# Kernel optimization log

Hardware: AMD Instinct MI355X
Metric: run time of the kernel (lower is better)

Reference implementation:

```python
import jax, jax.numpy as jnp
import numpy as np

N_SOURCE, N_TARGET, D, TFD, E = 100000, 50000, 128, 32, 640000


def setup_inputs() -> dict:
    key = jax.random.key(0)
    ks = jax.random.split(key, 6)
    x = jax.random.normal(ks[0], (N_SOURCE, D), dtype=jnp.float32)
    conv_weight = jax.random.normal(ks[1], (D, D), dtype=jnp.float32) / np.sqrt(D)
    conv_bias = jax.random.normal(ks[2], (D,), dtype=jnp.float32)
    target_feat = jax.random.normal(ks[3], (N_TARGET, TFD), dtype=jnp.float32)
    edge_weight = jax.random.uniform(ks[4], (E,), dtype=jnp.float32)
    inter_edge_index = jax.random.randint(ks[5], (2, E), 0, N_TARGET, dtype=jnp.int64)
    return {
        "x": x,
        "conv_weight": conv_weight,
        "conv_bias": conv_bias,
        "target_feat": target_feat,
        "edge_weight": edge_weight,
        "inter_edge_index": inter_edge_index,
    }


def reference(x, conv_weight, conv_bias, target_feat, edge_weight, inter_edge_index):
    n_source, _ = x.shape
    n_target = target_feat.shape[0]
    n_nodes = n_source + n_target  # padded graph: [source ; zero target rows]
    row = inter_edge_index[0]                 # source node ids
    col = inter_edge_index[1] + n_source      # shifted target node ids

    # GCN linear transform (zero-padded target rows stay zero, so only transform x)
    h = x @ conv_weight  # [n_source, D]

    # gcn_norm with remaining self-loops (fill value 1): deg = scatter_add over row + 1
    deg = jax.ops.segment_sum(edge_weight, row, num_segments=n_nodes) + 1.0
    dinv = jnp.where(deg > 0, jax.lax.rsqrt(deg), 0.0)
    norm = dinv[row] * edge_weight * dinv[col]  # [E]

    # message = norm * h[row]; aggregate (add) at targets. Self-loop messages on
    # targets are zero (zero-padded features), so they are omitted.
    msg = norm[:, None] * h[row]                       # [E, D]
    out_t = jax.ops.segment_sum(msg, col - n_source, num_segments=n_target)
    out_t = out_t + conv_bias

    out_t = jax.nn.relu(out_t)                         # if_relu=True
    return jnp.concatenate([out_t, jnp.abs(target_feat)], axis=1)  # mod='cat'
```

## Files before the change

### kernel.cpp

```cpp
#include <hip/hip_runtime.h>

#define N_SOURCE 100000
#define N_TARGET 50000
#define DIM 128
#define TFD 32
#define NE 640000
#define CAP 64

typedef __attribute__((ext_vector_type(8))) short short8;
typedef __attribute__((ext_vector_type(4))) float f32x4;

static constexpr size_t DEG_OFF   = 0;
static constexpr size_t CNT_OFF   = 262144;
static constexpr size_t XBF_OFF   = 524288;
static constexpr size_t WT_OFF    = 13324288;
static constexpr size_t PAIRS_OFF = 13357056;
static constexpr size_t ACC_OFF   = 26157056;

__device__ __forceinline__ unsigned short f2bf(float f) {
  unsigned u = __float_as_uint(f);
  return (unsigned short)((u + 0x7FFFu + ((u >> 16) & 1u)) >> 16);
}
__device__ __forceinline__ float bf2f(unsigned short u) {
  return __uint_as_float(((unsigned)u) << 16);
}

#define PREP_X_BLOCKS 3125
#define PREP_W_BLOCKS 8
#define EDGE_BLOCKS 2500
#define TOTAL_BLOCKS (PREP_X_BLOCKS + PREP_W_BLOCKS + EDGE_BLOCKS)

__global__ void prep_edges(const float* __restrict__ x, const float* __restrict__ W,
                           const int* __restrict__ row, const int* __restrict__ col,
                           const float* __restrict__ ew,
                           unsigned short* __restrict__ xbf, unsigned short* __restrict__ wt,
                           float* __restrict__ deg, int* __restrict__ cnt,
                           int* __restrict__ pairs) {
  int b = blockIdx.x, tid = threadIdx.x;
  if (b < PREP_X_BLOCKS) {
    size_t t = (size_t)b * 256 + tid;
    const float4* x4 = (const float4*)x;
    float4 u = x4[2 * t], v = x4[2 * t + 1];
    ((ushort4*)xbf)[2 * t]     = make_ushort4(f2bf(u.x), f2bf(u.y), f2bf(u.z), f2bf(u.w));
    ((ushort4*)xbf)[2 * t + 1] = make_ushort4(f2bf(v.x), f2bf(v.y), f2bf(v.z), f2bf(v.w));
  } else if (b < PREP_X_BLOCKS + PREP_W_BLOCKS) {
    int t = (b - PREP_X_BLOCKS) * 2048 + tid * 8;
    int n = t >> 7, k0 = t & 127;
#pragma unroll
    for (int j = 0; j < 8; ++j)
      wt[n * 128 + k0 + j] = f2bf(W[(k0 + j) * 128 + n]);
  } else {
    int e = (b - PREP_X_BLOCKS - PREP_W_BLOCKS) * 256 + tid;
    if (e >= NE) return;
    int c = col[e];
    int pos = atomicAdd(&cnt[c], 1);
    if (pos < CAP) pairs[(size_t)c * CAP + pos] = e;
    atomicAdd(&deg[row[e]], ew[e]);
  }
}

__global__ __launch_bounds__(256) void gather_agg(const int* __restrict__ cnt,
                                                  const int* __restrict__ pairs,
                                                  const float* __restrict__ deg,
                                                  const int* __restrict__ row,
                                                  const float* __restrict__ ew,
                                                  const unsigned short* __restrict__ xbf,
                                                  unsigned short* __restrict__ accb) {
  int g = blockIdx.x * 8 + (threadIdx.x >> 5);
  int lane = threadIdx.x & 31;
  if (g >= N_TARGET) return;
  int n = cnt[g];
  if (n > CAP) n = CAP;
  const int* __restrict__ pb = pairs + (size_t)g * CAP;
  float4 s = {0.f, 0.f, 0.f, 0.f};
  int e = 0;
  for (; e + 4 <= n; e += 4) {
    int4 q = *(const int4*)(pb + e);
    int r0 = row[q.x], r1 = row[q.y], r2 = row[q.z], r3 = row[q.w];
    float n0 = rsqrtf(deg[r0] + 1.0f) * ew[q.x];
    float n1 = rsqrtf(deg[r1] + 1.0f) * ew[q.y];
    float n2 = rsqrtf(deg[r2] + 1.0f) * ew[q.z];
    float n3 = rsqrtf(deg[r3] + 1.0f) * ew[q.w];
    ushort4 a0 = *(const ushort4*)(xbf + (size_t)r0 * DIM + lane * 4);
    ushort4 a1 = *(const ushort4*)(xbf + (size_t)r1 * DIM + lane * 4);
    ushort4 a2 = *(const ushort4*)(xbf + (size_t)r2 * DIM + lane * 4);
    ushort4 a3 = *(const ushort4*)(xbf + (size_t)r3 * DIM + lane * 4);
    s.x = fmaf(n0, bf2f(a0.x), s.x); s.y = fmaf(n0, bf2f(a0.y), s.y);
    s.z = fmaf(n0, bf2f(a0.z), s.z); s.w = fmaf(n0, bf2f(a0.w), s.w);
    s.x = fmaf(n1, bf2f(a1.x), s.x); s.y = fmaf(n1, bf2f(a1.y), s.y);
    s.z = fmaf(n1, bf2f(a1.z), s.z); s.w = fmaf(n1, bf2f(a1.w), s.w);
    s.x = fmaf(n2, bf2f(a2.x), s.x); s.y = fmaf(n2, bf2f(a2.y), s.y);
    s.z = fmaf(n2, bf2f(a2.z), s.z); s.w = fmaf(n2, bf2f(a2.w), s.w);
    s.x = fmaf(n3, bf2f(a3.x), s.x); s.y = fmaf(n3, bf2f(a3.y), s.y);
    s.z = fmaf(n3, bf2f(a3.z), s.z); s.w = fmaf(n3, bf2f(a3.w), s.w);
  }
  for (; e < n; ++e) {
    int pe = pb[e];
    int r = row[pe];
    float nr = rsqrtf(deg[r] + 1.0f) * ew[pe];
    ushort4 a = *(const ushort4*)(xbf + (size_t)r * DIM + lane * 4);
    s.x = fmaf(nr, bf2f(a.x), s.x); s.y = fmaf(nr, bf2f(a.y), s.y);
    s.z = fmaf(nr, bf2f(a.z), s.z); s.w = fmaf(nr, bf2f(a.w), s.w);
  }
  *(ushort4*)(accb + (size_t)g * DIM + lane * 4) =
      make_ushort4(f2bf(s.x), f2bf(s.y), f2bf(s.z), f2bf(s.w));
}

__global__ __launch_bounds__(256) void gemm_mfma(
    const unsigned short* __restrict__ accb, const unsigned short* __restrict__ wt,
    const float* __restrict__ bias, const float* __restrict__ tf,
    float* __restrict__ out) {
  const int tid = threadIdx.x;
  const int wave = tid >> 6;
  const int lane = tid & 63;
  const int row0 = blockIdx.x * 64;

  {
    const float4* tf4 = (const float4*)tf;
    int base = blockIdx.x * 512 + tid * 2;
#pragma unroll
    for (int q = 0; q < 2; ++q) {
      int t = base + q;
      int i = t >> 3, j = t & 7;
      if (i < N_TARGET) {
        float4 v = tf4[t];
        v.x = fabsf(v.x); v.y = fabsf(v.y); v.z = fabsf(v.z); v.w = fabsf(v.w);
        ((float4*)(out + (size_t)i * (DIM + TFD) + DIM))[j] = v;
      }
    }
  }

  const int mrow = row0 + wave * 16 + (lane & 15);
  const int kg = lane >> 4;
  short8 a[4];
  {
    const unsigned short* ap = accb + (size_t)mrow * DIM + kg * 8;
#pragma unroll
    for (int t = 0; t < 4; ++t) a[t] = *(const short8*)(ap + t * 32);
  }

  const int ncol = lane & 15;
  const int orow0 = row0 + wave * 16 + (lane >> 4) * 4;
#pragma unroll
  for (int c = 0; c < 8; ++c) {
    int n = c * 16 + ncol;
    f32x4 acc = {0.f, 0.f, 0.f, 0.f};
    const unsigned short* bp = wt + (size_t)n * DIM + kg * 8;
#pragma unroll
    for (int t = 0; t < 4; ++t) {
      short8 b = *(const short8*)(bp + t * 32);
      acc = __builtin_amdgcn_mfma_f32_16x16x32_bf16(a[t], b, acc, 0, 0, 0);
    }
    float bv = bias[n];
#pragma unroll
    for (int r = 0; r < 4; ++r) {
      int i = orow0 + r;
      if (i < N_TARGET)
        out[(size_t)i * (DIM + TFD) + n] = fmaxf(acc[r] + bv, 0.f);
    }
  }
}

extern "C" void kernel_launch(void* const* d_in, const int* in_sizes, int n_in,
                              void* d_out, int out_size, void* d_ws, size_t ws_size,
                              hipStream_t stream) {
  const float* x    = (const float*)d_in[0];
  const float* W    = (const float*)d_in[1];
  const float* bias = (const float*)d_in[2];
  const float* tf   = (const float*)d_in[3];
  const float* ew   = (const float*)d_in[4];
  const int*   eidx = (const int*)d_in[5];
  const int* row = eidx;
  const int* col = eidx + NE;
  float* out = (float*)d_out;

  float*          deg   = (float*)((char*)d_ws + DEG_OFF);
  int*            cnt   = (int*)((char*)d_ws + CNT_OFF);
  unsigned short* xbf   = (unsigned short*)((char*)d_ws + XBF_OFF);
  unsigned short* wt    = (unsigned short*)((char*)d_ws + WT_OFF);
  int*            pairs = (int*)((char*)d_ws + PAIRS_OFF);
  unsigned short* accb  = (unsigned short*)((char*)d_ws + ACC_OFF);

  hipMemsetAsync(d_ws, 0, XBF_OFF, stream);

  prep_edges<<<TOTAL_BLOCKS, 256, 0, stream>>>(x, W, row, col, ew, xbf, wt, deg, cnt, pairs);
  gather_agg<<<(N_TARGET + 7) / 8, 256, 0, stream>>>(cnt, pairs, deg, row, ew, xbf, accb);
  gemm_mfma<<<(N_TARGET + 63) / 64, 256, 0, stream>>>(accb, wt, bias, tf, out);
}
```

Baseline: 235.5 us.

## Fuse prep, gather and GEMM into one cooperative persistent kernel

```diff
diff --git a/kernel.cpp b/kernel.cpp
--- a/kernel.cpp
+++ b/kernel.cpp
@@ -1,4 +1,7 @@
 #include <hip/hip_runtime.h>
+#include <hip/hip_cooperative_groups.h>
+
+namespace cg = cooperative_groups;
 
 #define N_SOURCE 100000
 #define N_TARGET 50000
@@ -6,12 +9,15 @@
 #define TFD 32
 #define NE 640000
 #define CAP 64
+#define NBLK 1024
+#define NTHR 256
+#define NT (NBLK * NTHR)
 
 typedef __attribute__((ext_vector_type(8))) short short8;
 typedef __attribute__((ext_vector_type(4))) float f32x4;
 
 static constexpr size_t DEG_OFF   = 0;
-static constexpr size_t CNT_OFF   = 262144;
+static constexpr size_t CNT_OFF   = 204800;
 static constexpr size_t XBF_OFF   = 524288;
 static constexpr size_t WT_OFF    = 13324288;
 static constexpr size_t PAIRS_OFF = 13357056;
@@ -25,33 +31,28 @@
   return __uint_as_float(((unsigned)u) << 16);
 }
 
-#define PREP_X_BLOCKS 3125
-#define PREP_W_BLOCKS 8
-#define EDGE_BLOCKS 2500
-#define TOTAL_BLOCKS (PREP_X_BLOCKS + PREP_W_BLOCKS + EDGE_BLOCKS)
-
-__global__ void prep_edges(const float* __restrict__ x, const float* __restrict__ W,
-                           const int* __restrict__ row, const int* __restrict__ col,
-                           const float* __restrict__ ew,
-                           unsigned short* __restrict__ xbf, unsigned short* __restrict__ wt,
-                           float* __restrict__ deg, int* __restrict__ cnt,
-                           int* __restrict__ pairs) {
-  int b = blockIdx.x, tid = threadIdx.x;
-  if (b < PREP_X_BLOCKS) {
-    size_t t = (size_t)b * 256 + tid;
-    const float4* x4 = (const float4*)x;
+
+__device__ __forceinline__ void phase_prep_edges(
+    int gt, const float* __restrict__ x, const float* __restrict__ W,
+    const int* __restrict__ row, const int* __restrict__ col,
+    const float* __restrict__ ew, unsigned short* __restrict__ xbf,
+    unsigned short* __restrict__ wt, float* __restrict__ deg,
+    int* __restrict__ cnt, int* __restrict__ pairs) {
+  const float4* x4 = (const float4*)x;
+  ushort4* xb4 = (ushort4*)xbf;
+  for (int t = gt; t < 800000; t += NT) {
     float4 u = x4[2 * t], v = x4[2 * t + 1];
-    ((ushort4*)xbf)[2 * t]     = make_ushort4(f2bf(u.x), f2bf(u.y), f2bf(u.z), f2bf(u.w));
-    ((ushort4*)xbf)[2 * t + 1] = make_ushort4(f2bf(v.x), f2bf(v.y), f2bf(v.z), f2bf(v.w));
-  } else if (b < PREP_X_BLOCKS + PREP_W_BLOCKS) {
-    int t = (b - PREP_X_BLOCKS) * 2048 + tid * 8;
+    xb4[2 * t]     = make_ushort4(f2bf(u.x), f2bf(u.y), f2bf(u.z), f2bf(u.w));
+    xb4[2 * t + 1] = make_ushort4(f2bf(v.x), f2bf(v.y), f2bf(v.z), f2bf(v.w));
+  }
+  if (gt < 2048) {
+    int t = gt * 8;
     int n = t >> 7, k0 = t & 127;
 #pragma unroll
     for (int j = 0; j < 8; ++j)
       wt[n * 128 + k0 + j] = f2bf(W[(k0 + j) * 128 + n]);
-  } else {
-    int e = (b - PREP_X_BLOCKS - PREP_W_BLOCKS) * 256 + tid;
-    if (e >= NE) return;
+  }
+  for (int e = gt; e < NE; e += NT) {
     int c = col[e];
     int pos = atomicAdd(&cnt[c], 1);
     if (pos < CAP) pairs[(size_t)c * CAP + pos] = e;
@@ -59,106 +60,137 @@
   }
 }
 
-__global__ __launch_bounds__(256) void gather_agg(const int* __restrict__ cnt,
-                                                  const int* __restrict__ pairs,
-                                                  const float* __restrict__ deg,
-                                                  const int* __restrict__ row,
-                                                  const float* __restrict__ ew,
-                                                  const unsigned short* __restrict__ xbf,
-                                                  unsigned short* __restrict__ accb) {
-  int g = blockIdx.x * 8 + (threadIdx.x >> 5);
-  int lane = threadIdx.x & 31;
-  if (g >= N_TARGET) return;
-  int n = cnt[g];
-  if (n > CAP) n = CAP;
-  const int* __restrict__ pb = pairs + (size_t)g * CAP;
-  float4 s = {0.f, 0.f, 0.f, 0.f};
-  int e = 0;
-  for (; e + 4 <= n; e += 4) {
-    int4 q = *(const int4*)(pb + e);
-    int r0 = row[q.x], r1 = row[q.y], r2 = row[q.z], r3 = row[q.w];
-    float n0 = rsqrtf(deg[r0] + 1.0f) * ew[q.x];
-    float n1 = rsqrtf(deg[r1] + 1.0f) * ew[q.y];
-    float n2 = rsqrtf(deg[r2] + 1.0f) * ew[q.z];
-    float n3 = rsqrtf(deg[r3] + 1.0f) * ew[q.w];
-    ushort4 a0 = *(const ushort4*)(xbf + (size_t)r0 * DIM + lane * 4);
-    ushort4 a1 = *(const ushort4*)(xbf + (size_t)r1 * DIM + lane * 4);
-    ushort4 a2 = *(const ushort4*)(xbf + (size_t)r2 * DIM + lane * 4);
-    ushort4 a3 = *(const ushort4*)(xbf + (size_t)r3 * DIM + lane * 4);
-    s.x = fmaf(n0, bf2f(a0.x), s.x); s.y = fmaf(n0, bf2f(a0.y), s.y);
-    s.z = fmaf(n0, bf2f(a0.z), s.z); s.w = fmaf(n0, bf2f(a0.w), s.w);
-    s.x = fmaf(n1, bf2f(a1.x), s.x); s.y = fmaf(n1, bf2f(a1.y), s.y);
-    s.z = fmaf(n1, bf2f(a1.z), s.z); s.w = fmaf(n1, bf2f(a1.w), s.w);
-    s.x = fmaf(n2, bf2f(a2.x), s.x); s.y = fmaf(n2, bf2f(a2.y), s.y);
-    s.z = fmaf(n2, bf2f(a2.z), s.z); s.w = fmaf(n2, bf2f(a2.w), s.w);
-    s.x = fmaf(n3, bf2f(a3.x), s.x); s.y = fmaf(n3, bf2f(a3.y), s.y);
-    s.z = fmaf(n3, bf2f(a3.z), s.z); s.w = fmaf(n3, bf2f(a3.w), s.w);
-  }
-  for (; e < n; ++e) {
-    int pe = pb[e];
-    int r = row[pe];
-    float nr = rsqrtf(deg[r] + 1.0f) * ew[pe];
-    ushort4 a = *(const ushort4*)(xbf + (size_t)r * DIM + lane * 4);
-    s.x = fmaf(nr, bf2f(a.x), s.x); s.y = fmaf(nr, bf2f(a.y), s.y);
-    s.z = fmaf(nr, bf2f(a.z), s.z); s.w = fmaf(nr, bf2f(a.w), s.w);
-  }
-  *(ushort4*)(accb + (size_t)g * DIM + lane * 4) =
-      make_ushort4(f2bf(s.x), f2bf(s.y), f2bf(s.z), f2bf(s.w));
-}
-
-__global__ __launch_bounds__(256) void gemm_mfma(
-    const unsigned short* __restrict__ accb, const unsigned short* __restrict__ wt,
-    const float* __restrict__ bias, const float* __restrict__ tf,
-    float* __restrict__ out) {
-  const int tid = threadIdx.x;
-  const int wave = tid >> 6;
-  const int lane = tid & 63;
-  const int row0 = blockIdx.x * 64;
-
+__device__ __forceinline__ void phase_gather(
+    int gt, int lane, const int* __restrict__ cnt, const int* __restrict__ pairs,
+    const float* __restrict__ deg, const int* __restrict__ row,
+    const float* __restrict__ ew, const unsigned short* __restrict__ xbf,
+    unsigned short* __restrict__ accb) {
+  for (int g = (gt >> 5); g < N_TARGET; g += (NT >> 5)) {
+    int n = cnt[g];
+    if (n > CAP) n = CAP;
+    const int* __restrict__ pb = pairs + (size_t)g * CAP;
+    float4 s = {0.f, 0.f, 0.f, 0.f};
+    int e = 0;
+    for (; e + 4 <= n; e += 4) {
+      int4 q = *(const int4*)(pb + e);
+      int r0 = row[q.x], r1 = row[q.y], r2 = row[q.z], r3 = row[q.w];
+      float n0 = rsqrtf(deg[r0] + 1.0f) * ew[q.x];
+      float n1 = rsqrtf(deg[r1] + 1.0f) * ew[q.y];
+      float n2 = rsqrtf(deg[r2] + 1.0f) * ew[q.z];
+      float n3 = rsqrtf(deg[r3] + 1.0f) * ew[q.w];
+      ushort4 a0 = *(const ushort4*)(xbf + (size_t)r0 * DIM + lane * 4);
+      ushort4 a1 = *(const ushort4*)(xbf + (size_t)r1 * DIM + lane * 4);
+      ushort4 a2 = *(const ushort4*)(xbf + (size_t)r2 * DIM + lane * 4);
+      ushort4 a3 = *(const ushort4*)(xbf + (size_t)r3 * DIM + lane * 4);
+      s.x = fmaf(n0, bf2f(a0.x), s.x); s.y = fmaf(n0, bf2f(a0.y), s.y);
+      s.z = fmaf(n0, bf2f(a0.z), s.z); s.w = fmaf(n0, bf2f(a0.w), s.w);
+      s.x = fmaf(n1, bf2f(a1.x), s.x); s.y = fmaf(n1, bf2f(a1.y), s.y);
+      s.z = fmaf(n1, bf2f(a1.z), s.z); s.w = fmaf(n1, bf2f(a1.w), s.w);
+      s.x = fmaf(n2, bf2f(a2.x), s.x); s.y = fmaf(n2, bf2f(a2.y), s.y);
+      s.z = fmaf(n2, bf2f(a2.z), s.z); s.w = fmaf(n2, bf2f(a2.w), s.w);
+      s.x = fmaf(n3, bf2f(a3.x), s.x); s.y = fmaf(n3, bf2f(a3.y), s.y);
+      s.z = fmaf(n3, bf2f(a3.z), s.z); s.w = fmaf(n3, bf2f(a3.w), s.w);
+    }
+    for (; e < n; ++e) {
+      int pe = pb[e];
+      int r = row[pe];
+      float nr = rsqrtf(deg[r] + 1.0f) * ew[pe];
+      ushort4 a = *(const ushort4*)(xbf + (size_t)r * DIM + lane * 4);
+      s.x = fmaf(nr, bf2f(a.x), s.x); s.y = fmaf(nr, bf2f(a.y), s.y);
+      s.z = fmaf(nr, bf2f(a.z), s.z); s.w = fmaf(nr, bf2f(a.w), s.w);
+    }
+    *(ushort4*)(accb + (size_t)g * DIM + lane * 4) =
+        make_ushort4(f2bf(s.x), f2bf(s.y), f2bf(s.z), f2bf(s.w));
+  }
+}
+
+__device__ __forceinline__ void phase_gemm_tf(
+    int bid, int tid, int gt, const unsigned short* __restrict__ accb,
+    const unsigned short* __restrict__ wt, const float* __restrict__ bias,
+    const float* __restrict__ tf, float* __restrict__ out) {
   {
     const float4* tf4 = (const float4*)tf;
-    int base = blockIdx.x * 512 + tid * 2;
-#pragma unroll
-    for (int q = 0; q < 2; ++q) {
-      int t = base + q;
+    for (int t = gt; t < N_TARGET * (TFD / 4); t += NT) {
       int i = t >> 3, j = t & 7;
-      if (i < N_TARGET) {
-        float4 v = tf4[t];
-        v.x = fabsf(v.x); v.y = fabsf(v.y); v.z = fabsf(v.z); v.w = fabsf(v.w);
-        ((float4*)(out + (size_t)i * (DIM + TFD) + DIM))[j] = v;
+      float4 v = tf4[t];
+      v.x = fabsf(v.x); v.y = fabsf(v.y); v.z = fabsf(v.z); v.w = fabsf(v.w);
+      ((float4*)(out + (size_t)i * (DIM + TFD) + DIM))[j] = v;
+    }
+  }
+  if (bid < (N_TARGET + 63) / 64) {
+    const int wave = tid >> 6;
+    const int lane = tid & 63;
+    const int row0 = bid * 64;
+    const int mrow = row0 + wave * 16 + (lane & 15);
+    const int kg = lane >> 4;
+    short8 a[4];
+    const unsigned short* ap = accb + (size_t)mrow * DIM + kg * 8;
+#pragma unroll
+    for (int t = 0; t < 4; ++t) a[t] = *(const short8*)(ap + t * 32);
+
+    const int ncol = lane & 15;
+    const int orow0 = row0 + wave * 16 + (lane >> 4) * 4;
+#pragma unroll
+    for (int c = 0; c < 8; ++c) {
+      int n = c * 16 + ncol;
+      f32x4 acc = {0.f, 0.f, 0.f, 0.f};
+      const unsigned short* bp = wt + (size_t)n * DIM + kg * 8;
+#pragma unroll
+      for (int t = 0; t < 4; ++t) {
+        short8 b = *(const short8*)(bp + t * 32);
+        acc = __builtin_amdgcn_mfma_f32_16x16x32_bf16(a[t], b, acc, 0, 0, 0);
       }
-    }
-  }
-
-  const int mrow = row0 + wave * 16 + (lane & 15);
-  const int kg = lane >> 4;
-  short8 a[4];
-  {
-    const unsigned short* ap = accb + (size_t)mrow * DIM + kg * 8;
-#pragma unroll
-    for (int t = 0; t < 4; ++t) a[t] = *(const short8*)(ap + t * 32);
-  }
-
-  const int ncol = lane & 15;
-  const int orow0 = row0 + wave * 16 + (lane >> 4) * 4;
-#pragma unroll
-  for (int c = 0; c < 8; ++c) {
-    int n = c * 16 + ncol;
-    f32x4 acc = {0.f, 0.f, 0.f, 0.f};
-    const unsigned short* bp = wt + (size_t)n * DIM + kg * 8;
-#pragma unroll
-    for (int t = 0; t < 4; ++t) {
-      short8 b = *(const short8*)(bp + t * 32);
-      acc = __builtin_amdgcn_mfma_f32_16x16x32_bf16(a[t], b, acc, 0, 0, 0);
-    }
-    float bv = bias[n];
-#pragma unroll
-    for (int r = 0; r < 4; ++r) {
-      int i = orow0 + r;
-      if (i < N_TARGET)
-        out[(size_t)i * (DIM + TFD) + n] = fmaxf(acc[r] + bv, 0.f);
-    }
-  }
+      float bv = bias[n];
+#pragma unroll
+      for (int r = 0; r < 4; ++r) {
+        int i = orow0 + r;
+        if (i < N_TARGET)
+          out[(size_t)i * (DIM + TFD) + n] = fmaxf(acc[r] + bv, 0.f);
+      }
+    }
+  }
+}
+
+
+__global__ __launch_bounds__(NTHR, 4) void mega(
+    const float* x, const float* W, const float* bias, const float* tf,
+    const float* ew, const int* row, const int* col, float* out,
+    float* deg, int* cnt, unsigned short* xbf, unsigned short* wt,
+    int* pairs, unsigned short* accb) {
+  cg::grid_group grid = cg::this_grid();
+  const int tid = threadIdx.x;
+  const int bid = blockIdx.x;
+  const int gt = bid * NTHR + tid;
+
+  if (gt < N_TARGET) deg[gt] = 0.f;
+  else if (gt < 2 * N_TARGET) cnt[gt - N_TARGET] = 0;
+  grid.sync();
+
+  phase_prep_edges(gt, x, W, row, col, ew, xbf, wt, deg, cnt, pairs);
+  grid.sync();
+
+  phase_gather(gt, tid & 31, cnt, pairs, deg, row, ew, xbf, accb);
+  grid.sync();
+
+  phase_gemm_tf(bid, tid, gt, accb, wt, bias, tf, out);
+}
+
+
+__global__ __launch_bounds__(NTHR) void k_prep_edges(
+    const float* x, const float* W, const int* row, const int* col,
+    const float* ew, unsigned short* xbf, unsigned short* wt,
+    float* deg, int* cnt, int* pairs) {
+  phase_prep_edges(blockIdx.x * NTHR + threadIdx.x, x, W, row, col, ew, xbf, wt, deg, cnt, pairs);
+}
+__global__ __launch_bounds__(NTHR) void k_gather(
+    const int* cnt, const int* pairs, const float* deg, const int* row,
+    const float* ew, const unsigned short* xbf, unsigned short* accb) {
+  phase_gather(blockIdx.x * NTHR + threadIdx.x, threadIdx.x & 31, cnt, pairs, deg, row, ew, xbf, accb);
+}
+__global__ __launch_bounds__(NTHR) void k_gemm_tf(
+    const unsigned short* accb, const unsigned short* wt, const float* bias,
+    const float* tf, float* out) {
+  phase_gemm_tf(blockIdx.x, threadIdx.x, blockIdx.x * NTHR + threadIdx.x, accb, wt, bias, tf, out);
 }
 
 extern "C" void kernel_launch(void* const* d_in, const int* in_sizes, int n_in,
@@ -181,9 +213,14 @@
   int*            pairs = (int*)((char*)d_ws + PAIRS_OFF);
   unsigned short* accb  = (unsigned short*)((char*)d_ws + ACC_OFF);
 
-  hipMemsetAsync(d_ws, 0, XBF_OFF, stream);
-
-  prep_edges<<<TOTAL_BLOCKS, 256, 0, stream>>>(x, W, row, col, ew, xbf, wt, deg, cnt, pairs);
-  gather_agg<<<(N_TARGET + 7) / 8, 256, 0, stream>>>(cnt, pairs, deg, row, ew, xbf, accb);
-  gemm_mfma<<<(N_TARGET + 63) / 64, 256, 0, stream>>>(accb, wt, bias, tf, out);
-}
+  void* args[] = {&x, &W, &bias, &tf, &ew, &row, &col, &out,
+                  &deg, &cnt, &xbf, &wt, &pairs, &accb};
+  hipError_t rc = hipLaunchCooperativeKernel((void*)mega, dim3(NBLK), dim3(NTHR),
+                                             args, 0, stream);
+  if (rc != hipSuccess) {
+    hipMemsetAsync(d_ws, 0, CNT_OFF + 200000, stream);
+    k_prep_edges<<<NBLK, NTHR, 0, stream>>>(x, W, row, col, ew, xbf, wt, deg, cnt, pairs);
+    k_gather<<<NBLK, NTHR, 0, stream>>>(cnt, pairs, deg, row, ew, xbf, accb);
+    k_gemm_tf<<<NBLK, NTHR, 0, stream>>>(accb, wt, bias, tf, out);
+  }
+}
```

After: 611.7 us. 160% more time.
